# Performance work log

Hardware: AMD Instinct MI355X
Metric: run time of the kernel (lower is better)

The kernel has to match this reference:

```python
import jax, jax.numpy as jnp
import numpy as np

N = 50000          # nodes
E = 1_600_000      # edges (avg degree 32)
IN_DIM = 1024
HID = 32           # int(sqrt(IN_DIM))
OUT_DIMS = (2, 3)  # multi-task classifier heads


def setup_inputs() -> dict:
    key = jax.random.key(0)
    ks = jax.random.split(key, 16)
    x = jax.random.normal(ks[0], (N, IN_DIM), dtype=jnp.float32)
    adj_rows = jax.random.randint(ks[1], (E,), 0, N, dtype=jnp.int32)
    adj_cols = jax.random.randint(ks[2], (E,), 0, N, dtype=jnp.int32)
    adj_vals = jax.random.uniform(ks[3], (E,), dtype=jnp.float32) / 32.0  # ~normalized adj

    def xn(k, fan_in, fan_out, gain=0.75):  # xavier_normal with gain 3/4 (selu_xn)
        std = gain * np.sqrt(2.0 / (fan_in + fan_out))
        return jax.random.normal(k, (fan_in, fan_out), dtype=jnp.float32) * std

    w1 = xn(ks[4], IN_DIM, HID)
    w2 = xn(ks[5], HID, HID)
    w3 = xn(ks[6], HID, HID)
    b1 = jnp.zeros((HID,), jnp.float32)
    b2 = jnp.zeros((HID,), jnp.float32)
    b3 = jnp.zeros((HID,), jnp.float32)
    # clf heads: nn.Linear(HID, num_class), xavier_normal gain 1, zero bias
    clf_w0 = xn(ks[7], HID, OUT_DIMS[0], gain=1.0).T  # stored torch-style [out, in]
    clf_w1 = xn(ks[8], HID, OUT_DIMS[1], gain=1.0).T
    clf_b0 = jnp.zeros((OUT_DIMS[0],), jnp.float32)
    clf_b1 = jnp.zeros((OUT_DIMS[1],), jnp.float32)
    return {"x": x, "adj_rows": adj_rows, "adj_cols": adj_cols, "adj_vals": adj_vals,
            "w1": w1, "b1": b1, "w2": w2, "b2": b2, "w3": w3, "b3": b3,
            "clf_w0": clf_w0, "clf_b0": clf_b0, "clf_w1": clf_w1, "clf_b1": clf_b1}


def reference(x, adj_rows, adj_cols, adj_vals, w1, b1, w2, b2, w3, b3,
              clf_w0, clf_b0, clf_w1, clf_b1):
    def gcn_layer(h, w, b):
        support = h @ w                                   # [N, out]
        msgs = adj_vals[:, None] * support[adj_cols]      # gather along edges
        agg = jax.ops.segment_sum(msgs, adj_rows, num_segments=N)  # SpMM
        # eval mode: UniformDropout is identity; then SELU, then bias add
        return jax.nn.selu(agg) + b

    h = gcn_layer(x, w1, b1)
    h = gcn_layer(h, w2, b2)
    h = gcn_layer(h, w3, b3)
    out0 = h @ clf_w0.T + clf_b0   # [N, 2]
    out1 = h @ clf_w1.T + clf_b1   # [N, 3]
    return (out0, out1)
```

## Files before the change

kernel.cpp:

```cpp
#include <hip/hip_runtime.h>

#define IN_DIM 1024
#define HID 32
#define BSHIFT 5
#define BROWS 32
#define MAXB 1600
#define NBLKS 256
#define CAP 1536

typedef _Float16 h4 __attribute__((ext_vector_type(4)));

__device__ __forceinline__ float4 h4_to_f4(h4 v) {
    float4 r;
    r.x = (float)v.x; r.y = (float)v.y; r.z = (float)v.z; r.w = (float)v.w;
    return r;
}

__device__ __forceinline__ float selu_f(float x) {
    const float scale = 1.0507009873554805f;
    const float alpha = 1.6732632423543772f;
    return x > 0.f ? scale * x : scale * alpha * (expf(x) - 1.f);
}


__global__ __launch_bounds__(1024) void scatter_pad(const int* __restrict__ rows,
                                                    const int* __restrict__ cols,
                                                    const float* __restrict__ vals,
                                                    int E, int NB, int nchunk,
                                                    int* __restrict__ bcnt,
                                                    int2* __restrict__ epad) {
    __shared__ int lh[MAXB];
    __shared__ int lc[MAXB];
    int tid = threadIdx.x, blk = blockIdx.x;
    for (int b = tid; b < NB; b += 1024) lh[b] = 0;
    __syncthreads();
    int base = blk * nchunk;
    int end = base + nchunk; if (end > E) end = E;
    for (int i = base + tid; i < end; i += 1024)
        atomicAdd(&lh[rows[i] >> BSHIFT], 1);
    __syncthreads();
    for (int b = tid; b < NB; b += 1024) {
        int c = lh[b];
        lc[b] = (c > 0) ? atomicAdd(&bcnt[b], c) : 0;
    }
    __syncthreads();
    for (int i = base + tid; i < end; i += 1024) {
        int r = rows[i];
        int b = r >> BSHIFT;
        int p = atomicAdd(&lc[b], 1);
        if (p < CAP) {
            int2 pr;
            pr.x = ((r & (BROWS - 1)) << 18) | cols[i];
            pr.y = __float_as_int(vals[i]);
            epad[(size_t)b * CAP + p] = pr;
        }
    }
}


__global__ __launch_bounds__(256) void sort_pad(int2* __restrict__ epad,
                                                const int* __restrict__ bcnt,
                                                int NB,
                                                int2* __restrict__ rowptr2) {
    __shared__ int2 stage[CAP];
    __shared__ int cnt[32], startsh[32], cur[32];
    int b = blockIdx.x, tid = threadIdx.x;
    int n = bcnt[b]; if (n > CAP) n = CAP;
    int s0 = b * CAP;
    if (tid < 32) cnt[tid] = 0;
    __syncthreads();
    for (int i = tid; i < n; i += 256) {
        int2 pr = epad[s0 + i];
        stage[i] = pr;
        atomicAdd(&cnt[pr.x >> 18], 1);
    }
    __syncthreads();
    if (tid == 0) {
        int run = 0;
        #pragma unroll
        for (int k = 0; k < 32; ++k) { startsh[k] = run; run += cnt[k]; }
    }
    __syncthreads();
    if (tid < 32) {
        cur[tid] = startsh[tid];
        rowptr2[b * BROWS + tid] = make_int2(s0 + startsh[tid],
                                             s0 + startsh[tid] + cnt[tid]);
    }
    __syncthreads();
    for (int i = tid; i < n; i += 256) {
        int2 pr = stage[i];
        int p = atomicAdd(&cur[pr.x >> 18], 1);
        epad[s0 + p] = pr;
    }
}


#define BR 128
#define BK 64
#define XS_LD (BK + 4)

__global__ __launch_bounds__(256) void gemm1_kernel(const float* __restrict__ x,
                                                    const float* __restrict__ w,
                                                    _Float16* __restrict__ out, int N) {
    __shared__ float xs[BR * XS_LD];
    __shared__ float ws[BK * HID];
    int tid = threadIdx.x;
    int ct = tid & 7;
    int d0 = ct * 4;
    int rt = tid >> 3;
    int row0 = blockIdx.x * BR;

    float4 acc0 = {0,0,0,0}, acc1 = {0,0,0,0}, acc2 = {0,0,0,0}, acc3 = {0,0,0,0};

    for (int kc = 0; kc < IN_DIM; kc += BK) {
        #pragma unroll
        for (int j = 0; j < 8; ++j) {
            int linear = tid + j * 256;
            int rr = linear >> 4;
            int cc = linear & 15;
            int grow = row0 + rr;
            if (grow > N - 1) grow = N - 1;
            float4 t = *(const float4*)&x[(size_t)grow * IN_DIM + kc + cc * 4];
            *(float4*)&xs[rr * XS_LD + cc * 4] = t;
        }
        #pragma unroll
        for (int j = 0; j < 2; ++j) {
            int linear = tid + j * 256;
            int kk = linear >> 3;
            int dd = (linear & 7) * 4;
            float4 t = *(const float4*)&w[(kc + kk) * HID + dd];
            *(float4*)&ws[kk * HID + dd] = t;
        }
        __syncthreads();
        #pragma unroll
        for (int k4 = 0; k4 < BK / 4; ++k4) {
            float4 wv0 = *(const float4*)&ws[(k4 * 4 + 0) * HID + d0];
            float4 wv1 = *(const float4*)&ws[(k4 * 4 + 1) * HID + d0];
            float4 wv2 = *(const float4*)&ws[(k4 * 4 + 2) * HID + d0];
            float4 wv3 = *(const float4*)&ws[(k4 * 4 + 3) * HID + d0];
            float4 xv;
            #define GEMM_STEP(ACC, I) \
                xv = *(const float4*)&xs[(rt + 32 * I) * XS_LD + k4 * 4]; \
                ACC.x += xv.x * wv0.x; ACC.y += xv.x * wv0.y; ACC.z += xv.x * wv0.z; ACC.w += xv.x * wv0.w; \
                ACC.x += xv.y * wv1.x; ACC.y += xv.y * wv1.y; ACC.z += xv.y * wv1.z; ACC.w += xv.y * wv1.w; \
                ACC.x += xv.z * wv2.x; ACC.y += xv.z * wv2.y; ACC.z += xv.z * wv2.z; ACC.w += xv.z * wv2.w; \
                ACC.x += xv.w * wv3.x; ACC.y += xv.w * wv3.y; ACC.z += xv.w * wv3.z; ACC.w += xv.w * wv3.w;
            GEMM_STEP(acc0, 0)
            GEMM_STEP(acc1, 1)
            GEMM_STEP(acc2, 2)
            GEMM_STEP(acc3, 3)
            #undef GEMM_STEP
        }
        __syncthreads();
    }
    {
        int grow = row0 + rt;
        h4 o;
        o.x = (_Float16)acc0.x; o.y = (_Float16)acc0.y; o.z = (_Float16)acc0.z; o.w = (_Float16)acc0.w;
        if (grow < N)       *(h4*)&out[(size_t)grow * HID + d0] = o;
        grow += 32;
        o.x = (_Float16)acc1.x; o.y = (_Float16)acc1.y; o.z = (_Float16)acc1.z; o.w = (_Float16)acc1.w;
        if (grow < N)       *(h4*)&out[(size_t)grow * HID + d0] = o;
        grow += 32;
        o.x = (_Float16)acc2.x; o.y = (_Float16)acc2.y; o.z = (_Float16)acc2.z; o.w = (_Float16)acc2.w;
        if (grow < N)       *(h4*)&out[(size_t)grow * HID + d0] = o;
        grow += 32;
        o.x = (_Float16)acc3.x; o.y = (_Float16)acc3.y; o.z = (_Float16)acc3.z; o.w = (_Float16)acc3.w;
        if (grow < N)       *(h4*)&out[(size_t)grow * HID + d0] = o;
    }
}


__device__ __forceinline__ float4 spmm_row_f4(const h4* __restrict__ sup,
                                              const int2* __restrict__ edata,
                                              int e0, int e1, int l) {
    float4 a0 = {0.f,0.f,0.f,0.f}, a1 = a0, a2 = a0, a3 = a0;
    int e = e0;
    for (; e + 8 <= e1; e += 8) {
        int2 m0 = edata[e],   m1 = edata[e+1], m2 = edata[e+2], m3 = edata[e+3];
        int2 m4 = edata[e+4], m5 = edata[e+5], m6 = edata[e+6], m7 = edata[e+7];
        h4 g0 = sup[(size_t)(m0.x & 0x3FFFF) * 8 + l];
        h4 g1 = sup[(size_t)(m1.x & 0x3FFFF) * 8 + l];
        h4 g2 = sup[(size_t)(m2.x & 0x3FFFF) * 8 + l];
        h4 g3 = sup[(size_t)(m3.x & 0x3FFFF) * 8 + l];
        h4 g4 = sup[(size_t)(m4.x & 0x3FFFF) * 8 + l];
        h4 g5 = sup[(size_t)(m5.x & 0x3FFFF) * 8 + l];
        h4 g6 = sup[(size_t)(m6.x & 0x3FFFF) * 8 + l];
        h4 g7 = sup[(size_t)(m7.x & 0x3FFFF) * 8 + l];
        float v0 = __int_as_float(m0.y), v1 = __int_as_float(m1.y);
        float v2 = __int_as_float(m2.y), v3 = __int_as_float(m3.y);
        float v4 = __int_as_float(m4.y), v5 = __int_as_float(m5.y);
        float v6 = __int_as_float(m6.y), v7 = __int_as_float(m7.y);
        float4 f0 = h4_to_f4(g0), f1 = h4_to_f4(g1), f2 = h4_to_f4(g2), f3 = h4_to_f4(g3);
        float4 f4_ = h4_to_f4(g4), f5 = h4_to_f4(g5), f6 = h4_to_f4(g6), f7 = h4_to_f4(g7);
        a0.x += v0*f0.x; a0.y += v0*f0.y; a0.z += v0*f0.z; a0.w += v0*f0.w;
        a1.x += v1*f1.x; a1.y += v1*f1.y; a1.z += v1*f1.z; a1.w += v1*f1.w;
        a2.x += v2*f2.x; a2.y += v2*f2.y; a2.z += v2*f2.z; a2.w += v2*f2.w;
        a3.x += v3*f3.x; a3.y += v3*f3.y; a3.z += v3*f3.z; a3.w += v3*f3.w;
        a0.x += v4*f4_.x; a0.y += v4*f4_.y; a0.z += v4*f4_.z; a0.w += v4*f4_.w;
        a1.x += v5*f5.x; a1.y += v5*f5.y; a1.z += v5*f5.z; a1.w += v5*f5.w;
        a2.x += v6*f6.x; a2.y += v6*f6.y; a2.z += v6*f6.z; a2.w += v6*f6.w;
        a3.x += v7*f7.x; a3.y += v7*f7.y; a3.z += v7*f7.z; a3.w += v7*f7.w;
    }
    for (; e < e1; ++e) {
        int2 m0 = edata[e];
        h4 g0 = sup[(size_t)(m0.x & 0x3FFFF) * 8 + l];
        float v0 = __int_as_float(m0.y);
        float4 f0 = h4_to_f4(g0);
        a0.x += v0*f0.x; a0.y += v0*f0.y; a0.z += v0*f0.z; a0.w += v0*f0.w;
    }
    a0.x += a1.x + a2.x + a3.x;
    a0.y += a1.y + a2.y + a3.y;
    a0.z += a1.z + a2.z + a3.z;
    a0.w += a1.w + a2.w + a3.w;
    return a0;
}

__global__ __launch_bounds__(256) void spmm_mid_kernel(const h4* __restrict__ sup,
                                                       const int2* __restrict__ rowptr2,
                                                       const int2* __restrict__ edata,
                                                       int N,
                                                       const float* __restrict__ bias,
                                                       const float* __restrict__ Wn,
                                                       _Float16* __restrict__ out) {
    __shared__ float Wsh[HID * HID];
    __shared__ float hs[BROWS][36];
    int tid = threadIdx.x;
    int b = blockIdx.x;
    *(float4*)&Wsh[tid * 4] = ((const float4*)Wn)[tid];
    int g = tid >> 3, l = tid & 7;
    int row = b * BROWS + g;
    float4 acc = {0.f,0.f,0.f,0.f};
    if (row < N) {
        int2 ee = rowptr2[row];
        acc = spmm_row_f4(sup, edata, ee.x, ee.y, l);
    }
    float4 b4 = ((const float4*)bias)[l];
    float4 h;
    h.x = selu_f(acc.x) + b4.x;
    h.y = selu_f(acc.y) + b4.y;
    h.z = selu_f(acc.z) + b4.z;
    h.w = selu_f(acc.w) + b4.w;
    *(float4*)&hs[g][l * 4] = h;
    __syncthreads();
    int d = tid & 31;
    #pragma unroll
    for (int k = 0; k < 4; ++k) {
        int rl = (tid >> 5) + k * 8;
        int rrow = b * BROWS + rl;
        float o = 0.f;
        #pragma unroll
        for (int j = 0; j < HID; ++j) o += hs[rl][j] * Wsh[j * HID + d];
        if (rrow < N) out[(size_t)rrow * HID + d] = (_Float16)o;
    }
}

__global__ __launch_bounds__(256) void spmm_final_kernel(const h4* __restrict__ sup,
                                                         const int2* __restrict__ rowptr2,
                                                         const int2* __restrict__ edata,
                                                         int N,
                                                         const float* __restrict__ bias,
                                                         const float* __restrict__ cw0,
                                                         const float* __restrict__ cb0,
                                                         const float* __restrict__ cw1,
                                                         const float* __restrict__ cb1,
                                                         float* __restrict__ out) {
    __shared__ float hs[BROWS][36];
    int tid = threadIdx.x;
    int b = blockIdx.x;
    int g = tid >> 3, l = tid & 7;
    int row = b * BROWS + g;
    float4 acc = {0.f,0.f,0.f,0.f};
    if (row < N) {
        int2 ee = rowptr2[row];
        acc = spmm_row_f4(sup, edata, ee.x, ee.y, l);
    }
    float4 b4 = ((const float4*)bias)[l];
    float4 h;
    h.x = selu_f(acc.x) + b4.x;
    h.y = selu_f(acc.y) + b4.y;
    h.z = selu_f(acc.z) + b4.z;
    h.w = selu_f(acc.w) + b4.w;
    *(float4*)&hs[g][l * 4] = h;
    __syncthreads();
    if (tid < BROWS * 5) {
        int rl = tid / 5, t = tid % 5;
        int rrow = b * BROWS + rl;
        if (rrow < N) {
            if (t < 2) {
                float o = cb0[t];
                #pragma unroll
                for (int j = 0; j < HID; ++j) o += hs[rl][j] * cw0[t * HID + j];
                out[(size_t)rrow * 2 + t] = o;
            } else {
                int c = t - 2;
                float o = cb1[c];
                #pragma unroll
                for (int j = 0; j < HID; ++j) o += hs[rl][j] * cw1[c * HID + j];
                out[(size_t)N * 2 + (size_t)rrow * 3 + c] = o;
            }
        }
    }
}


extern "C" void kernel_launch(void* const* d_in, const int* in_sizes, int n_in,
                              void* d_out, int out_size, void* d_ws, size_t ws_size,
                              hipStream_t stream) {
    const float* x        = (const float*)d_in[0];
    const int*   adj_rows = (const int*)d_in[1];
    const int*   adj_cols = (const int*)d_in[2];
    const float* adj_vals = (const float*)d_in[3];
    const float* w1 = (const float*)d_in[4];
    const float* b1 = (const float*)d_in[5];
    const float* w2 = (const float*)d_in[6];
    const float* b2 = (const float*)d_in[7];
    const float* w3 = (const float*)d_in[8];
    const float* b3 = (const float*)d_in[9];
    const float* cw0 = (const float*)d_in[10];
    const float* cb0 = (const float*)d_in[11];
    const float* cw1 = (const float*)d_in[12];
    const float* cb1 = (const float*)d_in[13];

    int N = in_sizes[0] / IN_DIM;
    int E = in_sizes[1];
    int NB = (N + BROWS - 1) >> BSHIFT;
    int nchunk = (E + NBLKS - 1) / NBLKS;

    char* p = (char*)d_ws;
    _Float16* s_a = (_Float16*)p; p += (size_t)N * HID * sizeof(float);
    _Float16* s_b = (_Float16*)p; p += (size_t)N * HID * sizeof(float);
    int2*  epad    = (int2*)p; p += (size_t)NB * CAP * sizeof(int2);
    int*   bcnt    = (int*)p;  p += (size_t)NB * sizeof(int);
    int2*  rowptr2 = (int2*)p; p += (size_t)NB * BROWS * sizeof(int2);

    hipMemsetAsync(bcnt, 0, (size_t)NB * sizeof(int), stream);

    scatter_pad<<<NBLKS, 1024, 0, stream>>>(adj_rows, adj_cols, adj_vals, E, NB, nchunk,
                                            bcnt, epad);
    sort_pad<<<NB, 256, 0, stream>>>(epad, bcnt, NB, rowptr2);

    gemm1_kernel<<<(N + BR - 1) / BR, 256, 0, stream>>>(x, w1, s_a, N);
    spmm_mid_kernel<<<NB, 256, 0, stream>>>((const h4*)s_a, rowptr2, epad, N, b1, w2, s_b);
    spmm_mid_kernel<<<NB, 256, 0, stream>>>((const h4*)s_b, rowptr2, epad, N, b2, w3, s_a);
    spmm_final_kernel<<<NB, 256, 0, stream>>>((const h4*)s_a, rowptr2, epad, N,
                                              b3, cw0, cb0, cw1, cb1, (float*)d_out);
}
```

Before: 441.7 us.

## Fuse edge scatter with first GEMM and bucket sort with first SpMM layer

The edge bucketing scatter now runs as extra blocks inside the first dense GEMM launch, so the memory-bound GEMM and the atomic-heavy scatter can overlap in one grid. The per-bucket sort is fused into the first SpMM layer: each block sorts its bucket into shared memory and consumes the sorted edges directly, while still writing the sorted copy and row pointers back for the later layers. This removes two kernel launches and one re-read of the sorted edge list. In exchange, scatter blocks drop from 1024 to 256 threads, and the fused SpMM kernel uses much more shared memory, which may lower occupancy.

```diff
diff --git a/kernel.cpp b/kernel.cpp
--- a/kernel.cpp
+++ b/kernel.cpp
@@ -5,7 +5,7 @@
 #define BSHIFT 5
 #define BROWS 32
 #define MAXB 1600
-#define NBLKS 256
+#define SB 256
 #define CAP 1536
 
 typedef _Float16 h4 __attribute__((ext_vector_type(4)));
@@ -22,93 +22,56 @@
     return x > 0.f ? scale * x : scale * alpha * (expf(x) - 1.f);
 }
 
-
-__global__ __launch_bounds__(1024) void scatter_pad(const int* __restrict__ rows,
-                                                    const int* __restrict__ cols,
-                                                    const float* __restrict__ vals,
-                                                    int E, int NB, int nchunk,
-                                                    int* __restrict__ bcnt,
-                                                    int2* __restrict__ epad) {
-    __shared__ int lh[MAXB];
-    __shared__ int lc[MAXB];
-    int tid = threadIdx.x, blk = blockIdx.x;
-    for (int b = tid; b < NB; b += 1024) lh[b] = 0;
-    __syncthreads();
-    int base = blk * nchunk;
-    int end = base + nchunk; if (end > E) end = E;
-    for (int i = base + tid; i < end; i += 1024)
-        atomicAdd(&lh[rows[i] >> BSHIFT], 1);
-    __syncthreads();
-    for (int b = tid; b < NB; b += 1024) {
-        int c = lh[b];
-        lc[b] = (c > 0) ? atomicAdd(&bcnt[b], c) : 0;
-    }
-    __syncthreads();
-    for (int i = base + tid; i < end; i += 1024) {
-        int r = rows[i];
-        int b = r >> BSHIFT;
-        int p = atomicAdd(&lc[b], 1);
-        if (p < CAP) {
-            int2 pr;
-            pr.x = ((r & (BROWS - 1)) << 18) | cols[i];
-            pr.y = __float_as_int(vals[i]);
-            epad[(size_t)b * CAP + p] = pr;
-        }
-    }
-}
-
-
-__global__ __launch_bounds__(256) void sort_pad(int2* __restrict__ epad,
-                                                const int* __restrict__ bcnt,
-                                                int NB,
-                                                int2* __restrict__ rowptr2) {
-    __shared__ int2 stage[CAP];
-    __shared__ int cnt[32], startsh[32], cur[32];
-    int b = blockIdx.x, tid = threadIdx.x;
-    int n = bcnt[b]; if (n > CAP) n = CAP;
-    int s0 = b * CAP;
-    if (tid < 32) cnt[tid] = 0;
-    __syncthreads();
-    for (int i = tid; i < n; i += 256) {
-        int2 pr = epad[s0 + i];
-        stage[i] = pr;
-        atomicAdd(&cnt[pr.x >> 18], 1);
-    }
-    __syncthreads();
-    if (tid == 0) {
-        int run = 0;
-        #pragma unroll
-        for (int k = 0; k < 32; ++k) { startsh[k] = run; run += cnt[k]; }
-    }
-    __syncthreads();
-    if (tid < 32) {
-        cur[tid] = startsh[tid];
-        rowptr2[b * BROWS + tid] = make_int2(s0 + startsh[tid],
-                                             s0 + startsh[tid] + cnt[tid]);
-    }
-    __syncthreads();
-    for (int i = tid; i < n; i += 256) {
-        int2 pr = stage[i];
-        int p = atomicAdd(&cur[pr.x >> 18], 1);
-        epad[s0 + p] = pr;
-    }
-}
-
-
 #define BR 128
 #define BK 64
 #define XS_LD (BK + 4)
 
-__global__ __launch_bounds__(256) void gemm1_kernel(const float* __restrict__ x,
-                                                    const float* __restrict__ w,
-                                                    _Float16* __restrict__ out, int N) {
-    __shared__ float xs[BR * XS_LD];
-    __shared__ float ws[BK * HID];
+
+__global__ __launch_bounds__(256) void k1_scatter_gemm(
+        const int* __restrict__ rows, const int* __restrict__ cols,
+        const float* __restrict__ vals, int E, int NB, int nchunk,
+        int* __restrict__ bcnt, int2* __restrict__ epad,
+        const float* __restrict__ x, const float* __restrict__ w,
+        _Float16* __restrict__ out, int N) {
+    __shared__ alignas(16) char smem[BR * XS_LD * 4 + BK * HID * 4];
     int tid = threadIdx.x;
+
+    if (blockIdx.x < SB) {
+        int* lh = (int*)smem;
+        int* lc = lh + MAXB;
+        int blk = blockIdx.x;
+        for (int b = tid; b < NB; b += 256) lh[b] = 0;
+        __syncthreads();
+        int base = blk * nchunk;
+        int end = base + nchunk; if (end > E) end = E;
+        for (int i = base + tid; i < end; i += 256)
+            atomicAdd(&lh[rows[i] >> BSHIFT], 1);
+        __syncthreads();
+        for (int b = tid; b < NB; b += 256) {
+            int c = lh[b];
+            lc[b] = (c > 0) ? atomicAdd(&bcnt[b], c) : 0;
+        }
+        __syncthreads();
+        for (int i = base + tid; i < end; i += 256) {
+            int r = rows[i];
+            int b = r >> BSHIFT;
+            int p = atomicAdd(&lc[b], 1);
+            if (p < CAP) {
+                int2 pr;
+                pr.x = ((r & (BROWS - 1)) << 18) | cols[i];
+                pr.y = __float_as_int(vals[i]);
+                epad[(size_t)b * CAP + p] = pr;
+            }
+        }
+        return;
+    }
+
+    float* xs = (float*)smem;
+    float* ws = (float*)(smem + BR * XS_LD * 4);
     int ct = tid & 7;
     int d0 = ct * 4;
     int rt = tid >> 3;
-    int row0 = blockIdx.x * BR;
+    int row0 = (blockIdx.x - SB) * BR;
 
     float4 acc0 = {0,0,0,0}, acc1 = {0,0,0,0}, acc2 = {0,0,0,0}, acc3 = {0,0,0,0};
 
@@ -172,7 +135,7 @@
 
 
 __device__ __forceinline__ float4 spmm_row_f4(const h4* __restrict__ sup,
-                                              const int2* __restrict__ edata,
+                                              const int2* edata,
                                               int e0, int e1, int l) {
     float4 a0 = {0.f,0.f,0.f,0.f}, a1 = a0, a2 = a0, a3 = a0;
     int e = e0;
@@ -216,6 +179,81 @@
     return a0;
 }
 
+
+__global__ __launch_bounds__(256) void k2_sort_spmm(int2* __restrict__ epad,
+                                                    const int* __restrict__ bcnt,
+                                                    int N,
+                                                    const h4* __restrict__ sup,
+                                                    const float* __restrict__ bias,
+                                                    const float* __restrict__ Wn,
+                                                    _Float16* __restrict__ out,
+                                                    int2* __restrict__ rowptr2) {
+    __shared__ int2 stage[CAP];
+    __shared__ int2 sorted[CAP];
+    __shared__ int cnt[32], startsh[32], cur[32];
+    __shared__ float Wsh[HID * HID];
+    __shared__ float hs[BROWS][36];
+    int b = blockIdx.x, tid = threadIdx.x;
+    *(float4*)&Wsh[tid * 4] = ((const float4*)Wn)[tid];
+    int n = bcnt[b]; if (n > CAP) n = CAP;
+    int s0 = b * CAP;
+    if (tid < 32) cnt[tid] = 0;
+    __syncthreads();
+    for (int i = tid; i < n; i += 256) {
+        int2 pr = epad[s0 + i];
+        stage[i] = pr;
+        atomicAdd(&cnt[pr.x >> 18], 1);
+    }
+    __syncthreads();
+    if (tid == 0) {
+        int run = 0;
+        #pragma unroll
+        for (int k = 0; k < 32; ++k) { startsh[k] = run; run += cnt[k]; }
+    }
+    __syncthreads();
+    if (tid < 32) {
+        cur[tid] = startsh[tid];
+        rowptr2[b * BROWS + tid] = make_int2(s0 + startsh[tid],
+                                             s0 + startsh[tid] + cnt[tid]);
+    }
+    __syncthreads();
+    for (int i = tid; i < n; i += 256) {
+        int2 pr = stage[i];
+        int p = atomicAdd(&cur[pr.x >> 18], 1);
+        sorted[p] = pr;
+        epad[s0 + p] = pr;
+    }
+    __syncthreads();
+
+    int g = tid >> 3, l = tid & 7;
+    int row = b * BROWS + g;
+    float4 acc = {0.f,0.f,0.f,0.f};
+    if (row < N) {
+        int e0 = startsh[g];
+        int e1 = e0 + cnt[g];
+        acc = spmm_row_f4(sup, (const int2*)sorted, e0, e1, l);
+    }
+    float4 b4 = ((const float4*)bias)[l];
+    float4 h;
+    h.x = selu_f(acc.x) + b4.x;
+    h.y = selu_f(acc.y) + b4.y;
+    h.z = selu_f(acc.z) + b4.z;
+    h.w = selu_f(acc.w) + b4.w;
+    *(float4*)&hs[g][l * 4] = h;
+    __syncthreads();
+    int d = tid & 31;
+    #pragma unroll
+    for (int k = 0; k < 4; ++k) {
+        int rl = (tid >> 5) + k * 8;
+        int rrow = b * BROWS + rl;
+        float o = 0.f;
+        #pragma unroll
+        for (int j = 0; j < HID; ++j) o += hs[rl][j] * Wsh[j * HID + d];
+        if (rrow < N) out[(size_t)rrow * HID + d] = (_Float16)o;
+    }
+}
+
+
 __global__ __launch_bounds__(256) void spmm_mid_kernel(const h4* __restrict__ sup,
                                                        const int2* __restrict__ rowptr2,
                                                        const int2* __restrict__ edata,
@@ -325,7 +363,8 @@
     int N = in_sizes[0] / IN_DIM;
     int E = in_sizes[1];
     int NB = (N + BROWS - 1) >> BSHIFT;
-    int nchunk = (E + NBLKS - 1) / NBLKS;
+    int nchunk = (E + SB - 1) / SB;
+    int GB = (N + BR - 1) / BR;
 
     char* p = (char*)d_ws;
     _Float16* s_a = (_Float16*)p; p += (size_t)N * HID * sizeof(float);
@@ -336,12 +375,10 @@
 
     hipMemsetAsync(bcnt, 0, (size_t)NB * sizeof(int), stream);
 
-    scatter_pad<<<NBLKS, 1024, 0, stream>>>(adj_rows, adj_cols, adj_vals, E, NB, nchunk,
-                                            bcnt, epad);
-    sort_pad<<<NB, 256, 0, stream>>>(epad, bcnt, NB, rowptr2);
-
-    gemm1_kernel<<<(N + BR - 1) / BR, 256, 0, stream>>>(x, w1, s_a, N);
-    spmm_mid_kernel<<<NB, 256, 0, stream>>>((const h4*)s_a, rowptr2, epad, N, b1, w2, s_b);
+    k1_scatter_gemm<<<SB + GB, 256, 0, stream>>>(adj_rows, adj_cols, adj_vals, E, NB,
+                                                 nchunk, bcnt, epad, x, w1, s_a, N);
+    k2_sort_spmm<<<NB, 256, 0, stream>>>(epad, bcnt, N, (const h4*)s_a, b1, w2,
+                                         s_b, rowptr2);
     spmm_mid_kernel<<<NB, 256, 0, stream>>>((const h4*)s_b, rowptr2, epad, N, b2, w3, s_a);
     spmm_final_kernel<<<NB, 256, 0, stream>>>((const h4*)s_a, rowptr2, epad, N,
                                               b3, cw0, cb0, cw1, cb1, (float*)d_out);
```

After: 451.5 us. +2.2%, slower.

## Fuse per-block edge sort into first SpMM layer and halve GEMM K-tile

Applied to the files above, without the earlier changes.

The separate sort_pad kernel is removed. Its bucket sort now runs inside a new k2_sort_spmm kernel, which sorts each block's edges into shared memory and runs the first SpMM, SELU, bias and next-layer matmul straight from that sorted LDS copy. It still writes the sorted edges and row pointers back for the later layers. This saves one launch and one global reread of the edge list, at the cost of much more LDS per block (two CAP-sized int2 arrays plus weights), which may lower occupancy. The GEMM1 K-tile also shrinks from 64 to 32, which reduces shared memory but doubles the number of sync iterations.

```diff
diff --git a/kernel.cpp b/kernel.cpp
--- a/kernel.cpp
+++ b/kernel.cpp
@@ -58,45 +58,8 @@
 }
 
 
-__global__ __launch_bounds__(256) void sort_pad(int2* __restrict__ epad,
-                                                const int* __restrict__ bcnt,
-                                                int NB,
-                                                int2* __restrict__ rowptr2) {
-    __shared__ int2 stage[CAP];
-    __shared__ int cnt[32], startsh[32], cur[32];
-    int b = blockIdx.x, tid = threadIdx.x;
-    int n = bcnt[b]; if (n > CAP) n = CAP;
-    int s0 = b * CAP;
-    if (tid < 32) cnt[tid] = 0;
-    __syncthreads();
-    for (int i = tid; i < n; i += 256) {
-        int2 pr = epad[s0 + i];
-        stage[i] = pr;
-        atomicAdd(&cnt[pr.x >> 18], 1);
-    }
-    __syncthreads();
-    if (tid == 0) {
-        int run = 0;
-        #pragma unroll
-        for (int k = 0; k < 32; ++k) { startsh[k] = run; run += cnt[k]; }
-    }
-    __syncthreads();
-    if (tid < 32) {
-        cur[tid] = startsh[tid];
-        rowptr2[b * BROWS + tid] = make_int2(s0 + startsh[tid],
-                                             s0 + startsh[tid] + cnt[tid]);
-    }
-    __syncthreads();
-    for (int i = tid; i < n; i += 256) {
-        int2 pr = stage[i];
-        int p = atomicAdd(&cur[pr.x >> 18], 1);
-        epad[s0 + p] = pr;
-    }
-}
-
-
 #define BR 128
-#define BK 64
+#define BK 32
 #define XS_LD (BK + 4)
 
 __global__ __launch_bounds__(256) void gemm1_kernel(const float* __restrict__ x,
@@ -114,20 +77,18 @@
 
     for (int kc = 0; kc < IN_DIM; kc += BK) {
         #pragma unroll
-        for (int j = 0; j < 8; ++j) {
+        for (int j = 0; j < 4; ++j) {
             int linear = tid + j * 256;
-            int rr = linear >> 4;
-            int cc = linear & 15;
+            int rr = linear >> 3;
+            int cc = linear & 7;
             int grow = row0 + rr;
             if (grow > N - 1) grow = N - 1;
             float4 t = *(const float4*)&x[(size_t)grow * IN_DIM + kc + cc * 4];
             *(float4*)&xs[rr * XS_LD + cc * 4] = t;
         }
-        #pragma unroll
-        for (int j = 0; j < 2; ++j) {
-            int linear = tid + j * 256;
-            int kk = linear >> 3;
-            int dd = (linear & 7) * 4;
+        {
+            int kk = tid >> 3;
+            int dd = (tid & 7) * 4;
             float4 t = *(const float4*)&w[(kc + kk) * HID + dd];
             *(float4*)&ws[kk * HID + dd] = t;
         }
@@ -172,7 +133,7 @@
 
 
 __device__ __forceinline__ float4 spmm_row_f4(const h4* __restrict__ sup,
-                                              const int2* __restrict__ edata,
+                                              const int2* edata,
                                               int e0, int e1, int l) {
     float4 a0 = {0.f,0.f,0.f,0.f}, a1 = a0, a2 = a0, a3 = a0;
     int e = e0;
@@ -216,6 +177,81 @@
     return a0;
 }
 
+
+__global__ __launch_bounds__(256) void k2_sort_spmm(int2* __restrict__ epad,
+                                                    const int* __restrict__ bcnt,
+                                                    int N,
+                                                    const h4* __restrict__ sup,
+                                                    const float* __restrict__ bias,
+                                                    const float* __restrict__ Wn,
+                                                    _Float16* __restrict__ out,
+                                                    int2* __restrict__ rowptr2) {
+    __shared__ int2 stage[CAP];
+    __shared__ int2 sorted[CAP];
+    __shared__ int cnt[32], startsh[32], cur[32];
+    __shared__ float Wsh[HID * HID];
+    __shared__ float hs[BROWS][36];
+    int b = blockIdx.x, tid = threadIdx.x;
+    *(float4*)&Wsh[tid * 4] = ((const float4*)Wn)[tid];
+    int n = bcnt[b]; if (n > CAP) n = CAP;
+    int s0 = b * CAP;
+    if (tid < 32) cnt[tid] = 0;
+    __syncthreads();
+    for (int i = tid; i < n; i += 256) {
+        int2 pr = epad[s0 + i];
+        stage[i] = pr;
+        atomicAdd(&cnt[pr.x >> 18], 1);
+    }
+    __syncthreads();
+    if (tid == 0) {
+        int run = 0;
+        #pragma unroll
+        for (int k = 0; k < 32; ++k) { startsh[k] = run; run += cnt[k]; }
+    }
+    __syncthreads();
+    if (tid < 32) {
+        cur[tid] = startsh[tid];
+        rowptr2[b * BROWS + tid] = make_int2(s0 + startsh[tid],
+                                             s0 + startsh[tid] + cnt[tid]);
+    }
+    __syncthreads();
+    for (int i = tid; i < n; i += 256) {
+        int2 pr = stage[i];
+        int p = atomicAdd(&cur[pr.x >> 18], 1);
+        sorted[p] = pr;
+        epad[s0 + p] = pr;
+    }
+    __syncthreads();
+
+    int g = tid >> 3, l = tid & 7;
+    int row = b * BROWS + g;
+    float4 acc = {0.f,0.f,0.f,0.f};
+    if (row < N) {
+        int e0 = startsh[g];
+        int e1 = e0 + cnt[g];
+        acc = spmm_row_f4(sup, (const int2*)sorted, e0, e1, l);
+    }
+    float4 b4 = ((const float4*)bias)[l];
+    float4 h;
+    h.x = selu_f(acc.x) + b4.x;
+    h.y = selu_f(acc.y) + b4.y;
+    h.z = selu_f(acc.z) + b4.z;
+    h.w = selu_f(acc.w) + b4.w;
+    *(float4*)&hs[g][l * 4] = h;
+    __syncthreads();
+    int d = tid & 31;
+    #pragma unroll
+    for (int k = 0; k < 4; ++k) {
+        int rl = (tid >> 5) + k * 8;
+        int rrow = b * BROWS + rl;
+        float o = 0.f;
+        #pragma unroll
+        for (int j = 0; j < HID; ++j) o += hs[rl][j] * Wsh[j * HID + d];
+        if (rrow < N) out[(size_t)rrow * HID + d] = (_Float16)o;
+    }
+}
+
+
 __global__ __launch_bounds__(256) void spmm_mid_kernel(const h4* __restrict__ sup,
                                                        const int2* __restrict__ rowptr2,
                                                        const int2* __restrict__ edata,
@@ -338,10 +374,9 @@
 
     scatter_pad<<<NBLKS, 1024, 0, stream>>>(adj_rows, adj_cols, adj_vals, E, NB, nchunk,
                                             bcnt, epad);
-    sort_pad<<<NB, 256, 0, stream>>>(epad, bcnt, NB, rowptr2);
-
     gemm1_kernel<<<(N + BR - 1) / BR, 256, 0, stream>>>(x, w1, s_a, N);
-    spmm_mid_kernel<<<NB, 256, 0, stream>>>((const h4*)s_a, rowptr2, epad, N, b1, w2, s_b);
+    k2_sort_spmm<<<NB, 256, 0, stream>>>(epad, bcnt, N, (const h4*)s_a, b1, w2,
+                                         s_b, rowptr2);
     spmm_mid_kernel<<<NB, 256, 0, stream>>>((const h4*)s_b, rowptr2, epad, N, b2, w3, s_a);
     spmm_final_kernel<<<NB, 256, 0, stream>>>((const h4*)s_a, rowptr2, epad, N,
                                               b3, cw0, cb0, cw1, cb1, (float*)d_out);
```

New measurement: 448.8 us. About the same (+1.6%).
